# Performance work log

Measured on AMD Instinct MI355X. Metric: run time of the kernel, lower is better.

## Reference

```python
import jax, jax.numpy as jnp
import numpy as np

B_COMMITMENT = 1.0


def setup_inputs() -> dict:
    key = jax.random.key(0)
    k1, k2 = jax.random.split(key)
    inpt = jax.random.normal(k1, (16, 1024, 256), dtype=jnp.float32)
    emb_mtrx = jax.random.normal(k2, (256, 8192), dtype=jnp.float32) * 0.05
    return {"inpt": inpt, "emb_mtrx": emb_mtrx}


def reference(inpt, emb_mtrx):
    D = inpt.shape[-1]
    x = inpt.reshape(-1, D)  # [N, D]
    # squared L2 distance to every code: [N, K]
    dist = (
        jnp.sum(x * x, axis=1, keepdims=True)
        - 2.0 * (x @ emb_mtrx)
        + jnp.sum(emb_mtrx * emb_mtrx, axis=0, keepdims=True)
    )
    idx = jnp.argmin(dist, axis=1).reshape(inpt.shape[:-1])  # [B, T]
    q = jnp.take(emb_mtrx.T, idx, axis=0)  # [B, T, D] gather of nearest codes
    l_commitment = jnp.mean((jax.lax.stop_gradient(q) - inpt) ** 2)
    l_codebook = jnp.mean((q - jax.lax.stop_gradient(inpt)) ** 2)
    loss = B_COMMITMENT * l_commitment + l_codebook
    q_st = inpt + jax.lax.stop_gradient(q - inpt)  # straight-through
    return q_st, loss
```

## Files before the change

### kernel.cpp

```cpp
#include <hip/hip_runtime.h>
#include <hip/hip_bf16.h>
#include <cstdint>


typedef __bf16 bf16x8 __attribute__((ext_vector_type(8)));
typedef __bf16 bf16x4 __attribute__((ext_vector_type(4)));
typedef float  f32x16 __attribute__((ext_vector_type(16)));

#define N_ROWS  16384
#define N_CODES 8192
#define DDIM    256
#define NT      16
#define BUFB1   16384
#define BUFB3   32768
#define NMAX    8192
#define THETA   0.025f

#define STAGE16(gptr, lptr) __builtin_amdgcn_global_load_lds( \
    (const __attribute__((address_space(1))) void*)(gptr),    \
    (__attribute__((address_space(3))) void*)(lptr), 16, 0, 0)

#define SBAR() do { asm volatile("" ::: "memory"); \
                    __builtin_amdgcn_s_barrier();  \
                    asm volatile("" ::: "memory"); } while (0)
#define WAITVM(N) asm volatile("s_waitcnt vmcnt(" #N ")" ::: "memory")
#define LGKM0() do { asm volatile("s_waitcnt lgkmcnt(0)" ::: "memory"); \
                     __builtin_amdgcn_sched_barrier(0); } while (0)

__device__ __forceinline__ unsigned mapf(float f) {
  unsigned u = __float_as_uint(f);
  return (u & 0x80000000u) ? ~u : (u | 0x80000000u);
}
__device__ __forceinline__ float unmapf(unsigned u) {
  u = (u & 0x80000000u) ? (u & 0x7fffffffu) : ~u;
  return __uint_as_float(u);
}

__global__ void prep_x_k(const float* __restrict__ x,
                         __bf16* __restrict__ xhi, __bf16* __restrict__ xlo) {
  int i = blockIdx.x * 256 + threadIdx.x;
  float4 v = reinterpret_cast<const float4*>(x)[i];
  float a[4] = {v.x, v.y, v.z, v.w};
  bf16x4 h, l;
#pragma unroll
  for (int j = 0; j < 4; ++j) {
    __bf16 hh = (__bf16)a[j];
    h[j] = hh;
    l[j] = (__bf16)(a[j] - (float)hh);
  }
  reinterpret_cast<bf16x4*>(xhi)[i] = h;
  reinterpret_cast<bf16x4*>(xlo)[i] = l;
}

__global__ void prep_e_k(const float* __restrict__ emb,
                         __bf16* __restrict__ ehi, __bf16* __restrict__ elo) {
  __shared__ float tile[64][65];
  const int kb = blockIdx.x * 64, db = blockIdx.y * 64;
  const int t = threadIdx.x;
  const int tk = t & 63, td = t >> 6;
#pragma unroll
  for (int c = 0; c < 16; ++c) {
    int d = c * 4 + td;
    tile[d][tk] = emb[(size_t)(db + d) * N_CODES + kb + tk];
  }
  __syncthreads();
#pragma unroll
  for (int c = 0; c < 16; ++c) {
    int k = c * 4 + td;
    int d = tk;
    float v = tile[d][k];
    size_t o = (size_t)(kb + k) * DDIM + db + d;
    __bf16 h = (__bf16)v;
    ehi[o] = h;
    elo[o] = (__bf16)(v - (float)h);
  }
}

__global__ void enorm_k(const float* __restrict__ emb, float* __restrict__ enorm) {
  int k = blockIdx.x * 256 + threadIdx.x;
  float s = 0.f;
  for (int d = 0; d < DDIM; ++d) {
    float v = emb[(size_t)d * N_CODES + k];
    s += v * v;
  }
  enorm[k] = s;
}

__global__ __launch_bounds__(512, 2) void pass1_k(
    const __bf16* __restrict__ xhi, const __bf16* __restrict__ ehi,
    const float* __restrict__ enorm,
    unsigned long long* __restrict__ k2k, float* __restrict__ k2v) {
  __shared__ alignas(16) unsigned char smem[3][BUFB1];

  const int tid = threadIdx.x;
  const int wid = tid >> 6, lane = tid & 63;
  const int cg = wid >> 2, rg = wid & 3;
  const int l31 = lane & 31, lh = lane >> 5;

  const int orig = blockIdx.x;
  const int j = orig >> 3;
  const int bm = (orig & 7) * 8 + (j & 7);
  const int bn = j >> 3;

  const int cbase = bn * 256 + cg * 128 + lh * 4;
  f32x16 acc[4][2];
#pragma unroll
  for (int c = 0; c < 4; ++c) {
    f32x16 ci;
#pragma unroll
    for (int q = 0; q < 4; ++q)
#pragma unroll
      for (int r = 0; r < 4; ++r)
        ci[q * 4 + r] = -0.5f * enorm[cbase + c * 32 + q * 8 + r];
    acc[c][0] = ci; acc[c][1] = ci;
  }
  __builtin_amdgcn_sched_barrier(0);

  const size_t aoff = (size_t)(bm * 256 + wid * 32 + l31) * 512 + (size_t)lh * 16;
  const size_t boff = (size_t)(bn * 256 + wid * 32 + l31) * 512 + (size_t)lh * 16;
  const char* pxh = (const char*)xhi + aoff;
  const char* peh = (const char*)ehi + boff;
  const int dxh = wid * 1024, deh = 8192 + wid * 1024;

  const int xrd = rg * 2048 + lane * 16;
  const int erd = 8192 + cg * 4096 + lane * 16;

  unsigned char* b0 = &smem[0][0];
  unsigned char* b1 = &smem[1][0];
  unsigned char* b2 = &smem[2][0];

  STAGE16(pxh, b0 + dxh); STAGE16(peh, b0 + deh);
  STAGE16(pxh + 32, b1 + dxh); STAGE16(peh + 32, b1 + deh);
  WAITVM(2);
  SBAR();

#pragma unroll 1
  for (int t = 0; t < NT; ++t) {
    int s = t + 2; if (s >= NT) s -= NT;
    const size_t kb = (size_t)s * 32;

    bf16x8 ehf[4], xhf[2];
#pragma unroll
    for (int c = 0; c < 4; ++c) ehf[c] = *(const bf16x8*)(b0 + erd + c * 1024);
#pragma unroll
    for (int r = 0; r < 2; ++r) xhf[r] = *(const bf16x8*)(b0 + xrd + r * 1024);
    STAGE16(pxh + kb, b2 + dxh);
    STAGE16(peh + kb, b2 + deh);
    SBAR();
    LGKM0();
    __builtin_amdgcn_s_setprio(1);
#pragma unroll
    for (int c = 0; c < 4; ++c)
#pragma unroll
      for (int r = 0; r < 2; ++r)
        acc[c][r] = __builtin_amdgcn_mfma_f32_32x32x16_bf16(ehf[c], xhf[r], acc[c][r], 0, 0, 0);
    __builtin_amdgcn_s_setprio(0);
    WAITVM(2);
    SBAR();
    unsigned char* bt = b0; b0 = b1; b1 = b2; b2 = bt;
  }
  WAITVM(0);
  SBAR();

  unsigned long long* ek = (unsigned long long*)&smem[0][0];
  float* ev = (float*)(&smem[0][0] + 2048);
  const int rowl = rg * 64 + l31;

#pragma unroll
  for (int r = 0; r < 2; ++r) {
    float v1 = -3.4e38f, v2 = -3.4e38f;
    unsigned c1 = 0;
#pragma unroll
    for (int c = 0; c < 4; ++c)
#pragma unroll
      for (int q = 0; q < 4; ++q)
#pragma unroll
        for (int rr = 0; rr < 4; ++rr) {
          float v = acc[c][r][q * 4 + rr];
          unsigned cd = (unsigned)(cbase + c * 32 + q * 8 + rr);
          if (v > v1) { v2 = v1; v1 = v; c1 = cd; }
          else if (v > v2) v2 = v;
        }
    unsigned long long key =
        ((unsigned long long)mapf(v1) << 32) | (0xFFFFFFFFu ^ c1);
    unsigned klo = (unsigned)key, khi = (unsigned)(key >> 32);
    unsigned plo = __shfl_xor(klo, 32, 64), phi = __shfl_xor(khi, 32, 64);
    float pv1 = __shfl_xor(v1, 32, 64), pv2 = __shfl_xor(v2, 32, 64);
    unsigned long long pkey = ((unsigned long long)phi << 32) | plo;
    if (pkey > key) { v2 = fmaxf(v1, pv2); v1 = pv1; key = pkey; }
    else { v2 = fmaxf(pv1, v2); }
    SBAR();
    if (cg == 1 && lh == 0) { ek[rowl + r * 32] = key; ev[rowl + r * 32] = v2; }
    SBAR();
    if (cg == 0 && lh == 0) {
      unsigned long long pk = ek[rowl + r * 32];
      float ps2 = ev[rowl + r * 32];
      float nv2;
      if (pk > key) { nv2 = fmaxf(v1, ps2); key = pk; }
      else nv2 = fmaxf(unmapf((unsigned)(pk >> 32)), v2);
      const int grow = bm * 256 + rowl + r * 32;
      k2k[(size_t)bn * N_ROWS + grow] = key;
      k2v[(size_t)bn * N_ROWS + grow] = nv2;
    }
  }
}

__global__ void reduce_k(const unsigned long long* __restrict__ k2k,
                         const float* __restrict__ k2v,
                         unsigned long long* __restrict__ keys,
                         unsigned* __restrict__ counter,
                         int* __restrict__ idxlist) {
  const int row = blockIdx.x * 256 + threadIdx.x;
  unsigned long long k = k2k[row];
  float s2 = k2v[row];
#pragma unroll 1
  for (int p = 1; p < 32; ++p) {
    unsigned long long kk = k2k[(size_t)p * N_ROWS + row];
    float ss2 = k2v[(size_t)p * N_ROWS + row];
    if (kk > k) { s2 = fmaxf(unmapf((unsigned)(k >> 32)), ss2); k = kk; }
    else        { s2 = fmaxf(unmapf((unsigned)(kk >> 32)), s2); }
  }
  float v1 = unmapf((unsigned)(k >> 32));
  if (v1 - s2 >= THETA) {
    keys[row] = k;
  } else {
    keys[row] = 0;
    unsigned pos = atomicAdd(counter, 1u);
    if (pos < NMAX) idxlist[pos] = row;
    else keys[row] = k;
  }
}

__global__ void compact_k(const __bf16* __restrict__ xhi, const __bf16* __restrict__ xlo,
                          const int* __restrict__ idxlist, const unsigned* __restrict__ counter,
                          __bf16* __restrict__ xch, __bf16* __restrict__ xcl) {
  const unsigned b = blockIdx.x;
  if (b >= *counter) return;
  const int row = idxlist[b];
  const int lane = threadIdx.x;
  reinterpret_cast<uint2*>(xch)[(size_t)b * 64 + lane] =
      reinterpret_cast<const uint2*>(xhi)[(size_t)row * 64 + lane];
  reinterpret_cast<uint2*>(xcl)[(size_t)b * 64 + lane] =
      reinterpret_cast<const uint2*>(xlo)[(size_t)row * 64 + lane];
}

__global__ __launch_bounds__(512, 2) void rescue_k(
    const __bf16* __restrict__ xch, const __bf16* __restrict__ xcl,
    const __bf16* __restrict__ ehi, const __bf16* __restrict__ elo,
    const float* __restrict__ enorm, unsigned long long* __restrict__ keys,
    const int* __restrict__ idxlist, const unsigned* __restrict__ counter) {
  extern __shared__ __align__(16) unsigned char smem[];

  const int bm = blockIdx.x >> 5;
  const int bn = blockIdx.x & 31;
  const unsigned nf = *counter;
  const int tiles = (int)((nf + 255u) >> 8);
  if (bm >= tiles) return;

  const int tid = threadIdx.x;
  const int wid = tid >> 6, lane = tid & 63;
  const int cg = wid >> 2, rg = wid & 3;
  const int l31 = lane & 31, lh = lane >> 5;

  const int cbase = bn * 256 + cg * 128 + lh * 4;
  f32x16 acc[4][2];
#pragma unroll
  for (int c = 0; c < 4; ++c) {
    f32x16 ci;
#pragma unroll
    for (int q = 0; q < 4; ++q)
#pragma unroll
      for (int r = 0; r < 4; ++r)
        ci[q * 4 + r] = -0.5f * enorm[cbase + c * 32 + q * 8 + r];
    acc[c][0] = ci; acc[c][1] = ci;
  }
  __builtin_amdgcn_sched_barrier(0);

  const size_t aoff = (size_t)(bm * 256 + wid * 32 + l31) * 512 + (size_t)lh * 16;
  const size_t boff = (size_t)(bn * 256 + wid * 32 + l31) * 512 + (size_t)lh * 16;
  const char* pxh = (const char*)xch + aoff;
  const char* pxl = (const char*)xcl + aoff;
  const char* peh = (const char*)ehi + boff;
  const char* pel = (const char*)elo + boff;
  const int dxh = wid * 1024, dxl = 8192 + wid * 1024;
  const int deh = 16384 + wid * 1024, del = 24576 + wid * 1024;

  const int xrd = rg * 2048 + lane * 16;
  const int erd = 16384 + cg * 4096 + lane * 16;

  unsigned char* b0 = smem;
  unsigned char* b1 = smem + BUFB3;
  unsigned char* b2 = smem + 2 * BUFB3;

  STAGE16(pxh, b0 + dxh); STAGE16(peh, b0 + deh);
  STAGE16(pxl, b0 + dxl); STAGE16(pel, b0 + del);
  STAGE16(pxh + 32, b1 + dxh); STAGE16(peh + 32, b1 + deh);
  STAGE16(pxl + 32, b1 + dxl); STAGE16(pel + 32, b1 + del);
  WAITVM(4);
  SBAR();

#pragma unroll 1
  for (int t = 0; t < NT; ++t) {
    int s = t + 2; if (s >= NT) s -= NT;
    const size_t kb = (size_t)s * 32;

    bf16x8 ehf[4], xhf[2];
#pragma unroll
    for (int c = 0; c < 4; ++c) ehf[c] = *(const bf16x8*)(b0 + erd + c * 1024);
#pragma unroll
    for (int r = 0; r < 2; ++r) xhf[r] = *(const bf16x8*)(b0 + xrd + r * 1024);
    STAGE16(pxh + kb, b2 + dxh);
    STAGE16(peh + kb, b2 + deh);
    SBAR();
    LGKM0();
    __builtin_amdgcn_s_setprio(1);
#pragma unroll
    for (int c = 0; c < 4; ++c)
#pragma unroll
      for (int r = 0; r < 2; ++r)
        acc[c][r] = __builtin_amdgcn_mfma_f32_32x32x16_bf16(ehf[c], xhf[r], acc[c][r], 0, 0, 0);
    __builtin_amdgcn_s_setprio(0);
    SBAR();

    bf16x8 xlf[2];
#pragma unroll
    for (int r = 0; r < 2; ++r) xlf[r] = *(const bf16x8*)(b0 + 8192 + xrd + r * 1024);
    STAGE16(pxl + kb, b2 + dxl);
    SBAR();
    LGKM0();
    __builtin_amdgcn_s_setprio(1);
#pragma unroll
    for (int c = 0; c < 4; ++c)
#pragma unroll
      for (int r = 0; r < 2; ++r)
        acc[c][r] = __builtin_amdgcn_mfma_f32_32x32x16_bf16(ehf[c], xlf[r], acc[c][r], 0, 0, 0);
    __builtin_amdgcn_s_setprio(0);
    SBAR();

    bf16x8 elf[4];
#pragma unroll
    for (int c = 0; c < 4; ++c) elf[c] = *(const bf16x8*)(b0 + 8192 + erd + c * 1024);
    STAGE16(pel + kb, b2 + del);
    SBAR();
    LGKM0();
    __builtin_amdgcn_s_setprio(1);
#pragma unroll
    for (int c = 0; c < 4; ++c)
#pragma unroll
      for (int r = 0; r < 2; ++r)
        acc[c][r] = __builtin_amdgcn_mfma_f32_32x32x16_bf16(elf[c], xhf[r], acc[c][r], 0, 0, 0);
    __builtin_amdgcn_s_setprio(0);
    WAITVM(4);
    SBAR();

    unsigned char* bt = b0; b0 = b1; b1 = b2; b2 = bt;
  }
  WAITVM(0);

#pragma unroll
  for (int r = 0; r < 2; ++r) {
    float bv = -3.4e38f;
    unsigned bcode = 0;
#pragma unroll
    for (int c = 0; c < 4; ++c)
#pragma unroll
      for (int q = 0; q < 4; ++q)
#pragma unroll
        for (int rr = 0; rr < 4; ++rr) {
          float v = acc[c][r][q * 4 + rr];
          unsigned cd = (unsigned)(cbase + c * 32 + q * 8 + rr);
          if (v > bv) { bv = v; bcode = cd; }
        }
    unsigned long long key =
        ((unsigned long long)mapf(bv) << 32) | (0xFFFFFFFFu ^ bcode);
    unsigned olo = __shfl_xor((unsigned)key, 32, 64);
    unsigned ohi = __shfl_xor((unsigned)(key >> 32), 32, 64);
    unsigned long long okey = ((unsigned long long)ohi << 32) | olo;
    if (okey > key) key = okey;
    const int crow = bm * 256 + rg * 64 + r * 32 + l31;
    if (lane < 32 && crow < (int)nf)
      atomicMax(&keys[idxlist[crow]], key);
  }
}

__global__ void gather_k(const float* __restrict__ x,
                         const __bf16* __restrict__ ehi, const __bf16* __restrict__ elo,
                         const unsigned long long* __restrict__ keys,
                         float* __restrict__ qout, float* __restrict__ rowsum) {
  const int row = blockIdx.x;
  const int lane = threadIdx.x;
  const unsigned low = (unsigned)(keys[row] & 0xffffffffull);
  const int idx = (int)(~low);
  ushort4 h4 = reinterpret_cast<const ushort4*>(ehi + (size_t)idx * DDIM)[lane];
  ushort4 l4 = reinterpret_cast<const ushort4*>(elo + (size_t)idx * DDIM)[lane];
  float4 xv = reinterpret_cast<const float4*>(x + (size_t)row * DDIM)[lane];
  float4 q;
  q.x = __uint_as_float((unsigned)h4.x << 16) + __uint_as_float((unsigned)l4.x << 16);
  q.y = __uint_as_float((unsigned)h4.y << 16) + __uint_as_float((unsigned)l4.y << 16);
  q.z = __uint_as_float((unsigned)h4.z << 16) + __uint_as_float((unsigned)l4.z << 16);
  q.w = __uint_as_float((unsigned)h4.w << 16) + __uint_as_float((unsigned)l4.w << 16);
  reinterpret_cast<float4*>(qout + (size_t)row * DDIM)[lane] = q;
  float dx = q.x - xv.x, dy = q.y - xv.y, dz = q.z - xv.z, dw = q.w - xv.w;
  float s = dx * dx + dy * dy + dz * dz + dw * dw;
#pragma unroll
  for (int mk = 32; mk; mk >>= 1) s += __shfl_xor(s, mk, 64);
  if (lane == 0) rowsum[row] = s;
}

__global__ void loss_k(const float* __restrict__ rowsum, float* __restrict__ out) {
  __shared__ float sm[4];
  const int t = threadIdx.x;
  float s = 0.f;
  for (int j = t; j < N_ROWS; j += 256) s += rowsum[j];
#pragma unroll
  for (int mk = 32; mk; mk >>= 1) s += __shfl_xor(s, mk, 64);
  if ((t & 63) == 0) sm[t >> 6] = s;
  __syncthreads();
  if (t == 0) out[0] = 2.0f * (sm[0] + sm[1] + sm[2] + sm[3]) / (float)(N_ROWS * DDIM);
}

extern "C" void kernel_launch(void* const* d_in, const int* in_sizes, int n_in,
                              void* d_out, int out_size, void* d_ws, size_t ws_size,
                              hipStream_t stream) {
  const float* x   = (const float*)d_in[0];
  const float* emb = (const float*)d_in[1];
  float* qout = (float*)d_out;

  char* w = (char*)d_ws;
  unsigned long long* keys = (unsigned long long*)w;
  float* rowsum   = (float*)(w + 131072);
  unsigned* counter = (unsigned*)(w + 196608);
  int* idxlist    = (int*)(w + 197632);
  __bf16* xhi     = (__bf16*)(w + 262144);
  __bf16* xlo     = xhi + (size_t)N_ROWS * DDIM;
  __bf16* ehi     = xlo + (size_t)N_ROWS * DDIM;
  __bf16* elo     = ehi + (size_t)N_CODES * DDIM;
  float*  enorm   = (float*)(elo + (size_t)N_CODES * DDIM);
  char*   k2base  = (char*)(enorm + N_CODES);
  unsigned long long* k2k = (unsigned long long*)k2base;
  float*  k2v     = (float*)(k2base + 4194304);
  __bf16* xch     = (__bf16*)k2base;
  __bf16* xcl     = (__bf16*)(k2base + 4194304);

  hipFuncSetAttribute((const void*)rescue_k,
                      hipFuncAttributeMaxDynamicSharedMemorySize, 3 * BUFB3);

  hipMemsetAsync(counter, 0, sizeof(unsigned), stream);
  prep_x_k<<<4096, 256, 0, stream>>>(x, xhi, xlo);
  prep_e_k<<<dim3(N_CODES / 64, DDIM / 64), 256, 0, stream>>>(emb, ehi, elo);
  enorm_k<<<N_CODES / 256, 256, 0, stream>>>(emb, enorm);
  pass1_k<<<2048, 512, 0, stream>>>(xhi, ehi, enorm, k2k, k2v);
  reduce_k<<<N_ROWS / 256, 256, 0, stream>>>(k2k, k2v, keys, counter, idxlist);
  compact_k<<<NMAX, 64, 0, stream>>>(xhi, xlo, idxlist, counter, xch, xcl);
  rescue_k<<<(NMAX / 256) * 32, 512, 3 * BUFB3, stream>>>(
      xch, xcl, ehi, elo, enorm, keys, idxlist, counter);
  gather_k<<<N_ROWS, 64, 0, stream>>>(x, ehi, elo, keys, qout, rowsum);
  loss_k<<<1, 256, 0, stream>>>(rowsum, qout + (size_t)N_ROWS * DDIM);
}
```

Measured before the change: 239.4 us.

## Load x fragments directly to registers, stage only codebook tiles through LDS

```diff
diff --git a/kernel.cpp b/kernel.cpp
--- a/kernel.cpp
+++ b/kernel.cpp
@@ -11,10 +11,10 @@
 #define N_CODES 8192
 #define DDIM    256
 #define NT      16
-#define BUFB1   16384
+#define BUFB1   8192
 #define BUFB3   32768
 #define NMAX    8192
-#define THETA   0.025f
+#define THETA   0.020f
 
 #define STAGE16(gptr, lptr) __builtin_amdgcn_global_load_lds( \
     (const __attribute__((address_space(1))) void*)(gptr),    \
@@ -116,48 +116,50 @@
   }
   __builtin_amdgcn_sched_barrier(0);
 
-  const size_t aoff = (size_t)(bm * 256 + wid * 32 + l31) * 512 + (size_t)lh * 16;
   const size_t boff = (size_t)(bn * 256 + wid * 32 + l31) * 512 + (size_t)lh * 16;
-  const char* pxh = (const char*)xhi + aoff;
   const char* peh = (const char*)ehi + boff;
-  const int dxh = wid * 1024, deh = 8192 + wid * 1024;
-
-  const int xrd = rg * 2048 + lane * 16;
-  const int erd = 8192 + cg * 4096 + lane * 16;
-
-  unsigned char* b0 = &smem[0][0];
-  unsigned char* b1 = &smem[1][0];
-  unsigned char* b2 = &smem[2][0];
-
-  STAGE16(pxh, b0 + dxh); STAGE16(peh, b0 + deh);
-  STAGE16(pxh + 32, b1 + dxh); STAGE16(peh + 32, b1 + deh);
-  WAITVM(2);
+  const int deh = wid * 1024;
+
+  const char* pxg0 = (const char*)xhi +
+      (size_t)(bm * 256 + rg * 64 + 0 * 32 + l31) * 512 + (size_t)lh * 16;
+  const char* pxg1 = (const char*)xhi +
+      (size_t)(bm * 256 + rg * 64 + 1 * 32 + l31) * 512 + (size_t)lh * 16;
+
+  const int erd = cg * 4096 + lane * 16;
+
+  STAGE16(peh, &smem[0][0] + deh);
+  bf16x8 xc0 = *(const bf16x8*)(pxg0);
+  bf16x8 xc1 = *(const bf16x8*)(pxg1);
+  STAGE16(peh + 32, &smem[1][0] + deh);
+  WAITVM(1);
   SBAR();
 
 #pragma unroll 1
   for (int t = 0; t < NT; ++t) {
     int s = t + 2; if (s >= NT) s -= NT;
-    const size_t kb = (size_t)s * 32;
-
-    bf16x8 ehf[4], xhf[2];
-#pragma unroll
-    for (int c = 0; c < 4; ++c) ehf[c] = *(const bf16x8*)(b0 + erd + c * 1024);
-#pragma unroll
-    for (int r = 0; r < 2; ++r) xhf[r] = *(const bf16x8*)(b0 + xrd + r * 1024);
-    STAGE16(pxh + kb, b2 + dxh);
-    STAGE16(peh + kb, b2 + deh);
-    SBAR();
-    LGKM0();
+    int tn = t + 1; if (tn >= NT) tn -= NT;
+    const unsigned char* rb = &smem[t % 3][0];
+    unsigned char* wb = &smem[(t + 2) % 3][0];
+
+    bf16x8 xn0 = *(const bf16x8*)(pxg0 + tn * 32);
+    bf16x8 xn1 = *(const bf16x8*)(pxg1 + tn * 32);
+    STAGE16(peh + (size_t)s * 32, wb + deh);
+
+    bf16x8 ehf[4];
+#pragma unroll
+    for (int c = 0; c < 4; ++c) ehf[c] = *(const bf16x8*)(rb + erd + c * 1024);
+
     __builtin_amdgcn_s_setprio(1);
 #pragma unroll
-    for (int c = 0; c < 4; ++c)
-#pragma unroll
-      for (int r = 0; r < 2; ++r)
-        acc[c][r] = __builtin_amdgcn_mfma_f32_32x32x16_bf16(ehf[c], xhf[r], acc[c][r], 0, 0, 0);
+    for (int c = 0; c < 4; ++c) {
+      acc[c][0] = __builtin_amdgcn_mfma_f32_32x32x16_bf16(ehf[c], xc0, acc[c][0], 0, 0, 0);
+      acc[c][1] = __builtin_amdgcn_mfma_f32_32x32x16_bf16(ehf[c], xc1, acc[c][1], 0, 0, 0);
+    }
     __builtin_amdgcn_s_setprio(0);
-    WAITVM(2);
-    SBAR();
-    unsigned char* bt = b0; b0 = b1; b1 = b2; b2 = bt;
+
+    xc0 = xn0; xc1 = xn1;
+    WAITVM(3);
+    SBAR();
   }
   WAITVM(0);
   SBAR();
```

Result: slower. 291.4 us (+21.7%).
